# Performance work log

Measured on AMD Instinct MI355X. Metric: run time of the kernel, lower is better.

The kernel has to match this reference:

```python
import jax, jax.numpy as jnp
import numpy as np

D_MODEL = 2048
BOTTLENECK = 64
EPS = 1e-5  # torch LayerNorm default


def setup_inputs() -> dict:
    key = jax.random.key(0)
    k = jax.random.split(key, 7)
    x = jax.random.normal(k[0], (4, 4096, D_MODEL), dtype=jnp.float32)
    # LayerNorm params
    ln_gamma = jnp.ones((D_MODEL,), dtype=jnp.float32)
    ln_beta = jnp.zeros((D_MODEL,), dtype=jnp.float32)
    # down_proj: Linear(d_model -> bottleneck); torch weight shape [out, in]
    w_down = jax.random.normal(k[1], (BOTTLENECK, D_MODEL), dtype=jnp.float32) * (1.0 / np.sqrt(D_MODEL))
    b_down = jax.random.normal(k[2], (BOTTLENECK,), dtype=jnp.float32) * 0.01
    # up_proj: Linear(bottleneck -> d_model)
    w_up = jax.random.normal(k[3], (D_MODEL, BOTTLENECK), dtype=jnp.float32) * (1.0 / np.sqrt(BOTTLENECK))
    b_up = jax.random.normal(k[4], (D_MODEL,), dtype=jnp.float32) * 0.01
    return {"x": x, "ln_gamma": ln_gamma, "ln_beta": ln_beta,
            "w_down": w_down, "b_down": b_down, "w_up": w_up, "b_up": b_up}


def reference(x, ln_gamma, ln_beta, w_down, b_down, w_up, b_up):
    # adapter_layernorm_option == 'in': LayerNorm first
    mu = jnp.mean(x, axis=-1, keepdims=True)
    var = jnp.mean(jnp.square(x - mu), axis=-1, keepdims=True)
    xn = (x - mu) * jax.lax.rsqrt(var + EPS) * ln_gamma + ln_beta
    # down-proj -> ReLU -> up-proj (scale/dropout are never applied in forward)
    down = jnp.maximum(jnp.einsum('bsd,kd->bsk', xn, w_down) + b_down, 0.0)
    out = jnp.einsum('bsk,dk->bsd', down, w_up) + b_up
    return out
```

## Files before the change

kernel.cpp:

```cpp
#include <hip/hip_runtime.h>


typedef __attribute__((ext_vector_type(8))) short short8;
typedef __attribute__((ext_vector_type(4))) float f32x4;

#define D_MODEL 2048
#define BNECK   64
#define EPS     1e-5f

__device__ inline short f2bf(float f) {
    unsigned int u = __builtin_bit_cast(unsigned int, f);
    unsigned int r = (u + 0x7fffu + ((u >> 16) & 1u)) >> 16;
    return (short)r;
}
__device__ inline float bf2f(short s) {
    unsigned int u = ((unsigned int)(unsigned short)s) << 16;
    return __builtin_bit_cast(float, u);
}

__global__ __launch_bounds__(256) void prep_kernel(
    const float* __restrict__ w_down, const float* __restrict__ gamma,
    const float* __restrict__ beta,   const float* __restrict__ b_down,
    const float* __restrict__ w_up,
    short* __restrict__ wg_perm, short* __restrict__ wup_perm,
    float* __restrict__ s_out, float* __restrict__ c_out)
{
    __shared__ float rs[4], rc[4];
    int b = blockIdx.x;
    if (b < BNECK) {
        int n = b, nf = n >> 4;
        float ps = 0.f, pc = 0.f;
        for (int d = threadIdx.x; d < D_MODEL; d += 256) {
            float wv = w_down[n * D_MODEL + d];
            short h  = f2bf(wv * gamma[d]);
            int t = d >> 5, kg = (d >> 3) & 3, e = d & 7;
            int l = kg * 16 + (n & 15);
            wg_perm[(size_t)((t * 4 + nf) * 64 + l) * 8 + e] = h;
            ps += bf2f(h);
            pc  = fmaf(wv, beta[d], pc);
        }
        for (int o = 32; o > 0; o >>= 1) {
            ps += __shfl_down(ps, o, 64);
            pc += __shfl_down(pc, o, 64);
        }
        int wid = threadIdx.x >> 6, lane = threadIdx.x & 63;
        if (lane == 0) { rs[wid] = ps; rc[wid] = pc; }
        __syncthreads();
        if (threadIdx.x == 0) {
            s_out[n] = rs[0] + rs[1] + rs[2] + rs[3];
            c_out[n] = rc[0] + rc[1] + rc[2] + rc[3] + b_down[n];
        }
    } else {
        for (int j = (b - BNECK) * 256 + threadIdx.x; j < D_MODEL * BNECK;
             j += 64 * 256) {
            int d = j >> 6, kn = j & 63;
            int b16 = d >> 4, h2 = kn >> 5, e = kn & 7;
            int l = ((kn >> 3) & 3) * 16 + (d & 15);
            wup_perm[(size_t)((b16 * 2 + h2) * 64 + l) * 8 + e] = f2bf(w_up[j]);
        }
    }
}

struct W8 { short8 w[8]; };

__global__ __launch_bounds__(256, 4) void adapter_kernel(
    const float* __restrict__ x,    const float* __restrict__ b_up,
    const short* __restrict__ wg_perm, const short* __restrict__ wup_perm,
    const float* __restrict__ s_v,  const float* __restrict__ c_v,
    float* __restrict__ out)
{
    __shared__ __align__(16) char xstage[4][2][4096];
    __shared__ __align__(16) char tilebuf[2048];
    float (*red)[64][20] = reinterpret_cast<float(*)[64][20]>(&xstage[0][0][0]);

    const int wid  = threadIdx.x >> 6;
    const int lane = threadIdx.x & 63;
    const int r    = lane & 15;
    const int g    = lane >> 4;
    const int row0 = blockIdx.x * 16;
    const char* xbase = (const char*)x;
    const int swz = (r & 7) << 4;

    auto STAGE = [&](int c, int buf) {
#pragma unroll
        for (int i = 0; i < 4; ++i) {
            int rowl = i * 4 + g;
            const char* src = xbase +
                (((size_t)(row0 + rowl) * D_MODEL + wid * 512 + c * 64) << 2) +
                ((r * 16) ^ ((rowl & 7) << 4));
            __builtin_amdgcn_global_load_lds(
                (const __attribute__((address_space(1))) void*)src,
                (__attribute__((address_space(3))) void*)(&xstage[wid][buf][i * 1024]),
                16, 0, 0);
        }
    };
    auto LOADW = [&](int c) {
        W8 o;
        const short* p = wg_perm + ((size_t)(wid * 16 + c * 2) * 4) * 512
                       + lane * 8;
#pragma unroll
        for (int k = 0; k < 8; ++k) o.w[k] = *(const short8*)(p + k * 512);
        return o;
    };

    f32x4 acc[4];
#pragma unroll
    for (int nf = 0; nf < 4; ++nf) acc[nf] = (f32x4){0.f, 0.f, 0.f, 0.f};
    float sum = 0.f, sq = 0.f;

    STAGE(0, 0);
    W8 wcur = LOADW(0), wnxt;

#pragma unroll
    for (int c = 0; c < 8; ++c) {
        const int buf = c & 1;
        if (c < 7) {
            STAGE(c + 1, buf ^ 1);
            wnxt = LOADW(c + 1);
            asm volatile("s_waitcnt vmcnt(12)" ::: "memory");
        } else {
            asm volatile("s_waitcnt vmcnt(0)" ::: "memory");
        }
        const char* bp = &xstage[wid][buf][0];
#pragma unroll
        for (int kb = 0; kb < 2; ++kb) {
            int cb = kb * 128 + g * 32;
            f32x4 xa = *(const f32x4*)(bp + r * 256 + ( cb        ^ swz));
            f32x4 xb = *(const f32x4*)(bp + r * 256 + ((cb + 16)  ^ swz));
            sum += ((xa.x + xa.y) + (xa.z + xa.w)) +
                   ((xb.x + xb.y) + (xb.z + xb.w));
            sq = fmaf(xa.x, xa.x, sq); sq = fmaf(xa.y, xa.y, sq);
            sq = fmaf(xa.z, xa.z, sq); sq = fmaf(xa.w, xa.w, sq);
            sq = fmaf(xb.x, xb.x, sq); sq = fmaf(xb.y, xb.y, sq);
            sq = fmaf(xb.z, xb.z, sq); sq = fmaf(xb.w, xb.w, sq);
            short8 af;
            af[0] = f2bf(xa.x); af[1] = f2bf(xa.y);
            af[2] = f2bf(xa.z); af[3] = f2bf(xa.w);
            af[4] = f2bf(xb.x); af[5] = f2bf(xb.y);
            af[6] = f2bf(xb.z); af[7] = f2bf(xb.w);
            acc[0] = __builtin_amdgcn_mfma_f32_16x16x32_bf16(af, wcur.w[kb*4+0], acc[0], 0, 0, 0);
            acc[1] = __builtin_amdgcn_mfma_f32_16x16x32_bf16(af, wcur.w[kb*4+1], acc[1], 0, 0, 0);
            acc[2] = __builtin_amdgcn_mfma_f32_16x16x32_bf16(af, wcur.w[kb*4+2], acc[2], 0, 0, 0);
            acc[3] = __builtin_amdgcn_mfma_f32_16x16x32_bf16(af, wcur.w[kb*4+3], acc[3], 0, 0, 0);
        }
        if (c < 7) wcur = wnxt;
    }

    __syncthreads();
    float* myred = &red[wid][lane][0];
    *(f32x4*)(myred +  0) = acc[0];
    *(f32x4*)(myred +  4) = acc[1];
    *(f32x4*)(myred +  8) = acc[2];
    *(f32x4*)(myred + 12) = acc[3];
    myred[16] = sum; myred[17] = sq;
    __syncthreads();

    f32x4 accw = (f32x4){0.f, 0.f, 0.f, 0.f};
    float tsum = 0.f, tsq = 0.f;
#pragma unroll
    for (int w2 = 0; w2 < 4; ++w2) {
        const float* p = &red[w2][lane][0];
        accw += *(const f32x4*)(p + wid * 4);
        tsum += p[16]; tsq += p[17];
    }

    tsum += __shfl_xor(tsum, 16, 64); tsum += __shfl_xor(tsum, 32, 64);
    tsq  += __shfl_xor(tsq , 16, 64); tsq  += __shfl_xor(tsq , 32, 64);
    float mu_r   = tsum * (1.f / D_MODEL);
    float var    = tsq * (1.f / D_MODEL) - mu_r * mu_r;
    float rstd_r = rsqrtf(var + EPS);

    float mu_m[4], rs_m[4];
#pragma unroll
    for (int reg = 0; reg < 4; ++reg) {
        int m = g * 4 + reg;
        mu_m[reg] = __shfl(mu_r, m, 64);
        rs_m[reg] = __shfl(rstd_r, m, 64);
    }

    {
        int   n  = wid * 16 + r;
        float sn = s_v[n], cn = c_v[n];
#pragma unroll
        for (int reg = 0; reg < 4; ++reg) {
            int   m = g * 4 + reg;
            float v = fmaf(rs_m[reg], accw[reg] - mu_m[reg] * sn, cn);
            v = fmaxf(v, 0.f);
            *(short*)(tilebuf + ((m * 128 + n * 2) ^ ((m & 7) << 4))) = f2bf(v);
        }
    }
    __syncthreads();

    short8 bd0 = *(const short8*)(tilebuf + ((r * 128 +  0 + g * 16) ^ swz));
    short8 bd1 = *(const short8*)(tilebuf + ((r * 128 + 64 + g * 16) ^ swz));

    const short* wupl = wup_perm + lane * 8;
    float* outr = out + (size_t)(row0 + r) * D_MODEL;

#pragma unroll 4
    for (int i = 0; i < 32; ++i) {
        int b16 = wid * 32 + i;
        short8 a0 = *(const short8*)(wupl + (size_t)(b16 * 2 + 0) * 512);
        short8 a1 = *(const short8*)(wupl + (size_t)(b16 * 2 + 1) * 512);
        f32x4 o = (f32x4){0.f, 0.f, 0.f, 0.f};
        o = __builtin_amdgcn_mfma_f32_16x16x32_bf16(a0, bd0, o, 0, 0, 0);
        o = __builtin_amdgcn_mfma_f32_16x16x32_bf16(a1, bd1, o, 0, 0, 0);
        int dbase = b16 * 16;
        f32x4 bu = *(const f32x4*)(b_up + dbase + g * 4);
        o += bu;
        *(f32x4*)(outr + dbase + g * 4) = o;
    }
}

extern "C" void kernel_launch(void* const* d_in, const int* in_sizes, int n_in,
                              void* d_out, int out_size, void* d_ws, size_t ws_size,
                              hipStream_t stream) {
    const float* x      = (const float*)d_in[0];
    const float* gamma  = (const float*)d_in[1];
    const float* beta   = (const float*)d_in[2];
    const float* w_down = (const float*)d_in[3];
    const float* b_down = (const float*)d_in[4];
    const float* w_up   = (const float*)d_in[5];
    const float* b_up   = (const float*)d_in[6];
    float* out = (float*)d_out;

    char* ws = (char*)d_ws;
    short* wg_perm  = (short*)ws;
    short* wup_perm = (short*)(ws + 262144);
    float* s_v  = (float*)(ws + 524288);
    float* c_v  = (float*)(ws + 524544);

    prep_kernel<<<128, 256, 0, stream>>>(w_down, gamma, beta, b_down, w_up,
                                         wg_perm, wup_perm, s_v, c_v);
    adapter_kernel<<<1024, 256, 0, stream>>>(x, b_up, wg_perm, wup_perm,
                                             s_v, c_v, out);
}
```

Before: 76.15 us.

## Split down-proj across waves by output column instead of K slice

Each wave now computes one 16-column slice of the bottleneck over the full 2048-wide K, instead of a K quarter for all 64 columns. This removes the cross-wave LDS reduction of partial accumulators. The x tile is loaded cooperatively through registers into a shared double-buffered LDS tile, with a barrier every chunk and the row statistics computed during staging. Down-proj weights are re-laid out per column group, and up-proj weight loads are software-pipelined one iteration ahead. The cost is 32 block-wide barriers per tile and a loss of the direct global-to-LDS async loads.

```diff
diff --git a/kernel.cpp b/kernel.cpp
--- a/kernel.cpp
+++ b/kernel.cpp
@@ -7,6 +7,7 @@
 #define D_MODEL 2048
 #define BNECK   64
 #define EPS     1e-5f
+#define NCHUNK  32
 
 __device__ inline short f2bf(float f) {
     unsigned int u = __builtin_bit_cast(unsigned int, f);
@@ -35,7 +36,7 @@
             short h  = f2bf(wv * gamma[d]);
             int t = d >> 5, kg = (d >> 3) & 3, e = d & 7;
             int l = kg * 16 + (n & 15);
-            wg_perm[(size_t)((t * 4 + nf) * 64 + l) * 8 + e] = h;
+            wg_perm[(size_t)((nf * 64 + t) * 64 + l) * 8 + e] = h;
             ps += bf2f(h);
             pc  = fmaf(wv, beta[d], pc);
         }
@@ -61,122 +62,84 @@
     }
 }
 
-struct W8 { short8 w[8]; };
-
 __global__ __launch_bounds__(256, 4) void adapter_kernel(
     const float* __restrict__ x,    const float* __restrict__ b_up,
     const short* __restrict__ wg_perm, const short* __restrict__ wup_perm,
     const float* __restrict__ s_v,  const float* __restrict__ c_v,
     float* __restrict__ out)
 {
-    __shared__ __align__(16) char xstage[4][2][4096];
+    __shared__ __align__(16) char xbuf[2][4096];
     __shared__ __align__(16) char tilebuf[2048];
-    float (*red)[64][20] = reinterpret_cast<float(*)[64][20]>(&xstage[0][0][0]);
+    __shared__ float stats2[16][2];
 
     const int wid  = threadIdx.x >> 6;
     const int lane = threadIdx.x & 63;
     const int r    = lane & 15;
     const int g    = lane >> 4;
     const int row0 = blockIdx.x * 16;
-    const char* xbase = (const char*)x;
-    const int swz = (r & 7) << 4;
-
-    auto STAGE = [&](int c, int buf) {
-#pragma unroll
-        for (int i = 0; i < 4; ++i) {
-            int rowl = i * 4 + g;
-            const char* src = xbase +
-                (((size_t)(row0 + rowl) * D_MODEL + wid * 512 + c * 64) << 2) +
-                ((r * 16) ^ ((rowl & 7) << 4));
-            __builtin_amdgcn_global_load_lds(
-                (const __attribute__((address_space(1))) void*)src,
-                (__attribute__((address_space(3))) void*)(&xstage[wid][buf][i * 1024]),
-                16, 0, 0);
-        }
+    const int swz  = (r & 7) << 4;
+
+    const int srow = wid * 4 + g;
+    const int scol = r * 16;
+    const char* xsrc = (const char*)x
+        + ((size_t)(row0 + srow) * D_MODEL) * 4 + scol;
+    char* const swdst = &xbuf[0][0] + srow * 256 + (scol ^ ((srow & 7) << 4));
+
+    const short* wbase = wg_perm + (size_t)(wid * 64) * 512 + lane * 8;
+
+    f32x4  xr[4];
+    short8 wb[2][2];
+    f32x4  acc = (f32x4){0.f, 0.f, 0.f, 0.f};
+    float  ssum = 0.f, ssq = 0.f;
+
+    auto LDX = [&](int c) { return *(const f32x4*)(xsrc + c * 256); };
+    auto LDW = [&](int c, short8* w) {
+        w[0] = *(const short8*)(wbase + (size_t)(c * 2 + 0) * 512);
+        w[1] = *(const short8*)(wbase + (size_t)(c * 2 + 1) * 512);
     };
-    auto LOADW = [&](int c) {
-        W8 o;
-        const short* p = wg_perm + ((size_t)(wid * 16 + c * 2) * 4) * 512
-                       + lane * 8;
-#pragma unroll
-        for (int k = 0; k < 8; ++k) o.w[k] = *(const short8*)(p + k * 512);
-        return o;
+    auto STATS_WRITE = [&](int c, const f32x4& v) {
+        ssum += (v.x + v.y) + (v.z + v.w);
+        ssq = fmaf(v.x, v.x, ssq); ssq = fmaf(v.y, v.y, ssq);
+        ssq = fmaf(v.z, v.z, ssq); ssq = fmaf(v.w, v.w, ssq);
+        *(f32x4*)(swdst + (size_t)(c & 1) * 4096) = v;
     };
 
-    f32x4 acc[4];
-#pragma unroll
-    for (int nf = 0; nf < 4; ++nf) acc[nf] = (f32x4){0.f, 0.f, 0.f, 0.f};
-    float sum = 0.f, sq = 0.f;
-
-    STAGE(0, 0);
-    W8 wcur = LOADW(0), wnxt;
-
-#pragma unroll
-    for (int c = 0; c < 8; ++c) {
-        const int buf = c & 1;
-        if (c < 7) {
-            STAGE(c + 1, buf ^ 1);
-            wnxt = LOADW(c + 1);
-            asm volatile("s_waitcnt vmcnt(12)" ::: "memory");
-        } else {
-            asm volatile("s_waitcnt vmcnt(0)" ::: "memory");
-        }
-        const char* bp = &xstage[wid][buf][0];
+    xr[0] = LDX(0); xr[1] = LDX(1); xr[2] = LDX(2);
+    LDW(0, wb[0]);
+    STATS_WRITE(0, xr[0]);
+
+#pragma unroll
+    for (int c = 0; c < NCHUNK; ++c) {
+        if (c + 3 < NCHUNK) xr[(c + 3) & 3] = LDX(c + 3);
+        if (c + 1 < NCHUNK) LDW(c + 1, wb[(c + 1) & 1]);
+        asm volatile("s_waitcnt lgkmcnt(0)\n\ts_barrier" ::: "memory");
+        if (c + 1 < NCHUNK) STATS_WRITE(c + 1, xr[(c + 1) & 3]);
+
+        const char* bp = &xbuf[c & 1][0];
+        const short8* w = wb[c & 1];
 #pragma unroll
         for (int kb = 0; kb < 2; ++kb) {
             int cb = kb * 128 + g * 32;
             f32x4 xa = *(const f32x4*)(bp + r * 256 + ( cb        ^ swz));
             f32x4 xb = *(const f32x4*)(bp + r * 256 + ((cb + 16)  ^ swz));
-            sum += ((xa.x + xa.y) + (xa.z + xa.w)) +
-                   ((xb.x + xb.y) + (xb.z + xb.w));
-            sq = fmaf(xa.x, xa.x, sq); sq = fmaf(xa.y, xa.y, sq);
-            sq = fmaf(xa.z, xa.z, sq); sq = fmaf(xa.w, xa.w, sq);
-            sq = fmaf(xb.x, xb.x, sq); sq = fmaf(xb.y, xb.y, sq);
-            sq = fmaf(xb.z, xb.z, sq); sq = fmaf(xb.w, xb.w, sq);
             short8 af;
             af[0] = f2bf(xa.x); af[1] = f2bf(xa.y);
             af[2] = f2bf(xa.z); af[3] = f2bf(xa.w);
             af[4] = f2bf(xb.x); af[5] = f2bf(xb.y);
             af[6] = f2bf(xb.z); af[7] = f2bf(xb.w);
-            acc[0] = __builtin_amdgcn_mfma_f32_16x16x32_bf16(af, wcur.w[kb*4+0], acc[0], 0, 0, 0);
-            acc[1] = __builtin_amdgcn_mfma_f32_16x16x32_bf16(af, wcur.w[kb*4+1], acc[1], 0, 0, 0);
-            acc[2] = __builtin_amdgcn_mfma_f32_16x16x32_bf16(af, wcur.w[kb*4+2], acc[2], 0, 0, 0);
-            acc[3] = __builtin_amdgcn_mfma_f32_16x16x32_bf16(af, wcur.w[kb*4+3], acc[3], 0, 0, 0);
-        }
-        if (c < 7) wcur = wnxt;
-    }
-
+            acc = __builtin_amdgcn_mfma_f32_16x16x32_bf16(af, w[kb], acc, 0, 0, 0);
+        }
+    }
+
+#pragma unroll
+    for (int m = 1; m < 16; m <<= 1) {
+        ssum += __shfl_xor(ssum, m, 64);
+        ssq  += __shfl_xor(ssq , m, 64);
+    }
+    float mu   = ssum * (1.f / D_MODEL);
+    float rstd = rsqrtf(ssq * (1.f / D_MODEL) - mu * mu + EPS);
+    if (r == 0) { stats2[srow][0] = mu; stats2[srow][1] = rstd; }
     __syncthreads();
-    float* myred = &red[wid][lane][0];
-    *(f32x4*)(myred +  0) = acc[0];
-    *(f32x4*)(myred +  4) = acc[1];
-    *(f32x4*)(myred +  8) = acc[2];
-    *(f32x4*)(myred + 12) = acc[3];
-    myred[16] = sum; myred[17] = sq;
-    __syncthreads();
-
-    f32x4 accw = (f32x4){0.f, 0.f, 0.f, 0.f};
-    float tsum = 0.f, tsq = 0.f;
-#pragma unroll
-    for (int w2 = 0; w2 < 4; ++w2) {
-        const float* p = &red[w2][lane][0];
-        accw += *(const f32x4*)(p + wid * 4);
-        tsum += p[16]; tsq += p[17];
-    }
-
-    tsum += __shfl_xor(tsum, 16, 64); tsum += __shfl_xor(tsum, 32, 64);
-    tsq  += __shfl_xor(tsq , 16, 64); tsq  += __shfl_xor(tsq , 32, 64);
-    float mu_r   = tsum * (1.f / D_MODEL);
-    float var    = tsq * (1.f / D_MODEL) - mu_r * mu_r;
-    float rstd_r = rsqrtf(var + EPS);
-
-    float mu_m[4], rs_m[4];
-#pragma unroll
-    for (int reg = 0; reg < 4; ++reg) {
-        int m = g * 4 + reg;
-        mu_m[reg] = __shfl(mu_r, m, 64);
-        rs_m[reg] = __shfl(rstd_r, m, 64);
-    }
 
     {
         int   n  = wid * 16 + r;
@@ -184,7 +147,7 @@
 #pragma unroll
         for (int reg = 0; reg < 4; ++reg) {
             int   m = g * 4 + reg;
-            float v = fmaf(rs_m[reg], accw[reg] - mu_m[reg] * sn, cn);
+            float v = fmaf(stats2[m][1], acc[reg] - stats2[m][0] * sn, cn);
             v = fmaxf(v, 0.f);
             *(short*)(tilebuf + ((m * 128 + n * 2) ^ ((m & 7) << 4))) = f2bf(v);
         }
@@ -197,15 +160,24 @@
     const short* wupl = wup_perm + lane * 8;
     float* outr = out + (size_t)(row0 + r) * D_MODEL;
 
-#pragma unroll 4
+    short8 ua[2], ub[2];
+    {
+        int b16 = wid * 32;
+        ua[0] = *(const short8*)(wupl + (size_t)(b16 * 2 + 0) * 512);
+        ub[0] = *(const short8*)(wupl + (size_t)(b16 * 2 + 1) * 512);
+    }
+#pragma unroll
     for (int i = 0; i < 32; ++i) {
-        int b16 = wid * 32 + i;
-        short8 a0 = *(const short8*)(wupl + (size_t)(b16 * 2 + 0) * 512);
-        short8 a1 = *(const short8*)(wupl + (size_t)(b16 * 2 + 1) * 512);
+        int cur = i & 1;
+        if (i < 31) {
+            int b16 = wid * 32 + i + 1;
+            ua[cur ^ 1] = *(const short8*)(wupl + (size_t)(b16 * 2 + 0) * 512);
+            ub[cur ^ 1] = *(const short8*)(wupl + (size_t)(b16 * 2 + 1) * 512);
+        }
         f32x4 o = (f32x4){0.f, 0.f, 0.f, 0.f};
-        o = __builtin_amdgcn_mfma_f32_16x16x32_bf16(a0, bd0, o, 0, 0, 0);
-        o = __builtin_amdgcn_mfma_f32_16x16x32_bf16(a1, bd1, o, 0, 0, 0);
-        int dbase = b16 * 16;
+        o = __builtin_amdgcn_mfma_f32_16x16x32_bf16(ua[cur], bd0, o, 0, 0, 0);
+        o = __builtin_amdgcn_mfma_f32_16x16x32_bf16(ub[cur], bd1, o, 0, 0, 0);
+        int dbase = (wid * 32 + i) * 16;
         f32x4 bu = *(const f32x4*)(b_up + dbase + g * 4);
         o += bu;
         *(f32x4*)(outr + dbase + g * 4) = o;
```

New measurement: 67.99 us. 1.12x faster.
